# Kernel tuning notes

Measured on AMD Instinct MI355X. Metric: run time of the kernel, lower is better.

Reference implementation:

```python
import jax, jax.numpy as jnp
import numpy as np

HEADS = 8
DIM_HEAD = 32
SCALE = DIM_HEAD ** (-0.5)


def setup_inputs() -> dict:
    key = jax.random.key(0)
    k1, k2, k3, k4 = jax.random.split(key, 4)
    x = jax.random.normal(k1, (16, 256, 64, 64), dtype=jnp.float32)
    # conv 1x1 weights stored as [out_ch, in_ch]
    w_qkv = jax.random.normal(k2, (3 * HEADS * DIM_HEAD, 256), dtype=jnp.float32) * 0.05
    w_out = jax.random.normal(k3, (256, HEADS * DIM_HEAD), dtype=jnp.float32) * 0.05
    b_out = jax.random.normal(k4, (256,), dtype=jnp.float32) * 0.05
    return {"x": x, "w_qkv": w_qkv, "w_out": w_out, "b_out": b_out}


def reference(x, w_qkv, w_out, b_out):
    b, c, h, w = x.shape
    n = h * w
    # 1x1 conv (no bias) == channel matmul
    qkv = jnp.einsum('bchw,oc->bohw', x, w_qkv)            # [b, 3*H*D, h, w]
    qkv = qkv.reshape(b, 3, HEADS, DIM_HEAD, n)            # chunk then 'b (h c) xy'
    q, k, v = qkv[:, 0], qkv[:, 1], qkv[:, 2]              # [b, H, D, n]
    q = jax.nn.softmax(q, axis=-2) * SCALE                 # softmax over channel dim d
    k = jax.nn.softmax(k, axis=-1)                         # softmax over spatial n
    context = jnp.einsum('bhdn,bhen->bhde', k, v)          # [b, H, D, D]
    out = jnp.einsum('bhde,bhdn->bhen', context, q)        # [b, H, D, n]
    out = out.reshape(b, HEADS * DIM_HEAD, h, w)
    # 1x1 conv with bias
    return jnp.einsum('bchw,oc->bohw', out, w_out) + b_out[None, :, None, None]
```

## Files before the change

kernel.cpp:

```cpp
#include <hip/hip_runtime.h>
#include <cstddef>
#include <cstdint>

#define NN 4096
#define CIN 256
#define CQKV 768
#define NBATCH 16
#define QSCALE 0.17677669529663687f

typedef short s16x8 __attribute__((ext_vector_type(8)));
typedef float f32x4 __attribute__((ext_vector_type(4)));

__device__ __forceinline__ float bf2f(unsigned short u) {
    unsigned int x = ((unsigned int)u) << 16;
    return __builtin_bit_cast(float, x);
}
__device__ __forceinline__ unsigned short f2bf(float f) {
    unsigned int u = __builtin_bit_cast(unsigned int, f);
    return (unsigned short)((u + 0x7fffu + ((u >> 16) & 1u)) >> 16);
}
__device__ __forceinline__ void glds16(const void* gsrc, void* lds) {
    __builtin_amdgcn_global_load_lds(
        (const __attribute__((address_space(1))) unsigned int*)gsrc,
        (__attribute__((address_space(3))) unsigned int*)lds,
        16, 0, 0);
}

__global__ __launch_bounds__(256)
void xpose(const float* __restrict__ x, unsigned short* __restrict__ xT)
{
    const int b = blockIdx.z;
    const int n0 = blockIdx.x * 64, c0 = blockIdx.y * 64;
    __shared__ float xs[64][65];
    const int t = threadIdx.x;
    const float* xb = x + (size_t)b * CIN * NN;
#pragma unroll
    for (int p = 0; p < 4; ++p) {
        const int row = p * 16 + (t >> 4);
        const int col = (t & 15) * 4;
        const float4 v = *reinterpret_cast<const float4*>(
            &xb[(size_t)(c0 + row) * NN + n0 + col]);
        xs[col + 0][row] = v.x; xs[col + 1][row] = v.y;
        xs[col + 2][row] = v.z; xs[col + 3][row] = v.w;
    }
    __syncthreads();
    const int n = t >> 2, cch = (t & 3) * 16;
    unsigned short arr[16];
#pragma unroll
    for (int e = 0; e < 16; ++e) arr[e] = f2bf(xs[n][cch + e]);
    unsigned short* dst = xT + ((size_t)b * NN + n0 + n) * 256 + c0 + cch;
    *reinterpret_cast<s16x8*>(&dst[0]) = *reinterpret_cast<s16x8*>(&arr[0]);
    *reinterpret_cast<s16x8*>(&dst[8]) = *reinterpret_cast<s16x8*>(&arr[8]);
}

__global__ __launch_bounds__(256)
void wcvt(const float* __restrict__ w, unsigned short* __restrict__ wb)
{
    const int i = (blockIdx.x * 256 + threadIdx.x) * 4;
    const float4 v = *reinterpret_cast<const float4*>(&w[i]);
    unsigned short a[4] = { f2bf(v.x), f2bf(v.y), f2bf(v.z), f2bf(v.w) };
    *reinterpret_cast<ushort2*>(&wb[i])     = *reinterpret_cast<ushort2*>(&a[0]);
    *reinterpret_cast<ushort2*>(&wb[i + 2]) = *reinterpret_cast<ushort2*>(&a[2]);
}

__device__ __forceinline__ void gemm_core64(const unsigned short* __restrict__ Ab,
                                            const unsigned short* __restrict__ Bb,
                                            int m0, int n0, char* smem,
                                            f32x4 (&acc)[4][4])
{
    const int t = threadIdx.x;
    const int lane = t & 63, w = t >> 6;
    const int lr = lane & 15, lq = lane >> 4;
    const int wr = (w >> 1) * 64, wc = (w & 1) * 64;
    const int srow = t >> 3;
    const int schunk = (t & 7) ^ (srow & 7);
    const int wq = w << 10;
    const int xr = lr & 7;

    char* A0 = smem;          char* B0 = smem + 16384;
    char* A1 = smem + 32768;  char* B1 = smem + 49152;

#define STG(bufA, bufB, k0)                                                     \
    { _Pragma("unroll") for (int i = 0; i < 4; ++i)                             \
        glds16(Ab + (size_t)(m0 + i*32 + srow)*256 + (k0) + schunk*8,           \
               (bufA) + i*4096 + wq);                                           \
      _Pragma("unroll") for (int i = 0; i < 4; ++i)                             \
        glds16(Bb + (size_t)(n0 + i*32 + srow)*256 + (k0) + schunk*8,           \
               (bufB) + i*4096 + wq); }

#define CMP(bufA, bufB)                                                         \
    { s16x8 af[4][2], bfr[4][2];                                                \
      _Pragma("unroll") for (int m = 0; m < 4; ++m) {                           \
        const char* rp = (bufA) + (wr + m*16 + lr)*128;                         \
        af[m][0] = *(const s16x8*)(rp + (((0*4 + lq) ^ xr) << 4));              \
        af[m][1] = *(const s16x8*)(rp + (((1*4 + lq) ^ xr) << 4)); }            \
      _Pragma("unroll") for (int n = 0; n < 4; ++n) {                           \
        const char* rp = (bufB) + (wc + n*16 + lr)*128;                         \
        bfr[n][0] = *(const s16x8*)(rp + (((0*4 + lq) ^ xr) << 4));             \
        bfr[n][1] = *(const s16x8*)(rp + (((1*4 + lq) ^ xr) << 4)); }           \
      _Pragma("unroll") for (int m = 0; m < 4; ++m)                             \
      _Pragma("unroll") for (int n = 0; n < 4; ++n) {                           \
        acc[m][n] = __builtin_amdgcn_mfma_f32_16x16x32_bf16(af[m][0], bfr[n][0], acc[m][n], 0, 0, 0); \
        acc[m][n] = __builtin_amdgcn_mfma_f32_16x16x32_bf16(af[m][1], bfr[n][1], acc[m][n], 0, 0, 0); }}

    STG(A0, B0, 0);
    __syncthreads();
    STG(A1, B1, 64);
    CMP(A0, B0);
    __syncthreads();
    STG(A0, B0, 128);
    CMP(A1, B1);
    __syncthreads();
    STG(A1, B1, 192);
    CMP(A0, B0);
    __syncthreads();
    CMP(A1, B1);
#undef STG
#undef CMP
}

__global__ __launch_bounds__(256, 2)
void qkv_fused(const unsigned short* __restrict__ wb,
               const unsigned short* __restrict__ xT,
               unsigned short* __restrict__ qT,
               float* __restrict__ ctx_part,
               float* __restrict__ z_part)
{
    __shared__ __align__(16) char smem[65536];
    const int nt = blockIdx.x;
    const int ty = blockIdx.y;
    const int b  = blockIdx.z;
    const int t = threadIdx.x;
    const int lane = t & 63, w = t >> 6;
    const int lr = lane & 15, lq = lane >> 4;
    const int wr = (w >> 1) * 64, wc = (w & 1) * 64;
    const int n0 = nt * 128;

    if (ty < 2) {
        const int m0 = ty * 128;
        const unsigned short* Bb = xT + (size_t)b * NN * 256;
        f32x4 acc[4][4] = {};
        gemm_core64(wb, Bb, m0, n0, smem, acc);

        __syncthreads();
        unsigned short (*qs)[136] = (unsigned short (*)[136])smem;
#pragma unroll
        for (int n = 0; n < 4; ++n) {
            const int col = wc + n * 16 + lr;
#pragma unroll
            for (int hp = 0; hp < 2; ++hp) {
                float mx = -1e30f;
#pragma unroll
                for (int u = 0; u < 2; ++u)
#pragma unroll
                    for (int r = 0; r < 4; ++r)
                        mx = fmaxf(mx, acc[hp * 2 + u][n][r]);
                mx = fmaxf(mx, __shfl_xor(mx, 16));
                mx = fmaxf(mx, __shfl_xor(mx, 32));
                float er[2][4];
                float s = 0.f;
#pragma unroll
                for (int u = 0; u < 2; ++u)
#pragma unroll
                    for (int r = 0; r < 4; ++r) {
                        er[u][r] = __expf(acc[hp * 2 + u][n][r] - mx);
                        s += er[u][r];
                    }
                s += __shfl_xor(s, 16);
                s += __shfl_xor(s, 32);
                const float inv = QSCALE / s;
#pragma unroll
                for (int u = 0; u < 2; ++u) {
                    ushort4 pk;
                    pk.x = f2bf(er[u][0] * inv);
                    pk.y = f2bf(er[u][1] * inv);
                    pk.z = f2bf(er[u][2] * inv);
                    pk.w = f2bf(er[u][3] * inv);
                    *(ushort4*)&qs[col][wr + (hp * 2 + u) * 16 + lq * 4] = pk;
                }
            }
        }
        __syncthreads();
        const int nl = t >> 1, half = t & 1;
        const unsigned short* src = &qs[nl][half * 64];
        unsigned short* dst = qT + ((size_t)b * NN + n0 + nl) * 256 + m0 + half * 64;
#pragma unroll
        for (int i = 0; i < 8; ++i)
            *(s16x8*)(dst + i * 8) = *(const s16x8*)(src + i * 8);
    } else {
        const int g = ty - 2;
        const unsigned short* An = xT + ((size_t)b * NN + (size_t)n0) * 256;

        f32x4 acc[4][4] = {};
        gemm_core64(An, wb, 0, 256 + g * 128, smem, acc);

        unsigned int ekpk[4][4][2];
        float zl[4] = {0.f, 0.f, 0.f, 0.f};
#pragma unroll
        for (int m = 0; m < 4; ++m)
#pragma unroll
            for (int nn = 0; nn < 4; ++nn) {
                const unsigned short u0 = f2bf(__expf(acc[m][nn][0]));
                const unsigned short u1 = f2bf(__expf(acc[m][nn][1]));
                const unsigned short u2 = f2bf(__expf(acc[m][nn][2]));
                const unsigned short u3 = f2bf(__expf(acc[m][nn][3]));
                zl[nn] += bf2f(u0) + bf2f(u1) + bf2f(u2) + bf2f(u3);
                ekpk[m][nn][0] = (unsigned int)u0 | ((unsigned int)u1 << 16);
                ekpk[m][nn][1] = (unsigned int)u2 | ((unsigned int)u3 << 16);
            }
#pragma unroll
        for (int nn = 0; nn < 4; ++nn) {
            zl[nn] += __shfl_xor(zl[nn], 16);
            zl[nn] += __shfl_xor(zl[nn], 32);
        }
        const float zv = (lq == 0) ? zl[0] : (lq == 1) ? zl[1] : (lq == 2) ? zl[2] : zl[3];
        z_part[((((size_t)(b * 32 + nt)) * 2 + g) * 2 + (w >> 1)) * 128 + wc + lane] = zv;

#pragma unroll
        for (int m = 0; m < 4; ++m)
#pragma unroll
            for (int nn = 0; nn < 4; ++nn) acc[m][nn] = (f32x4){0.f, 0.f, 0.f, 0.f};
        gemm_core64(An, wb, 0, 512 + g * 128, smem, acc);

        __syncthreads();
#pragma unroll
        for (int m = 0; m < 4; ++m)
#pragma unroll
            for (int nn = 0; nn < 4; ++nn) {
                const int col = wc + nn * 16 + lr;
                const int swz = (col & 7) << 4;
                const int rowb = (wr + m * 16 + lq * 4) * 2;
                *(unsigned int*)(smem + ((col * 256 + rowb) ^ swz))       = ekpk[m][nn][0];
                *(unsigned int*)(smem + ((col * 256 + rowb + 4) ^ swz))   = ekpk[m][nn][1];
                const unsigned int vp0 = (unsigned int)f2bf(acc[m][nn][0])
                                       | ((unsigned int)f2bf(acc[m][nn][1]) << 16);
                const unsigned int vp1 = (unsigned int)f2bf(acc[m][nn][2])
                                       | ((unsigned int)f2bf(acc[m][nn][3]) << 16);
                *(unsigned int*)(smem + 32768 + ((col * 256 + rowb) ^ swz))     = vp0;
                *(unsigned int*)(smem + 32768 + ((col * 256 + rowb + 4) ^ swz)) = vp1;
            }
        __syncthreads();

        f32x4 cacc[2][2] = {};
#pragma unroll
        for (int ks = 0; ks < 4; ++ks) {
            s16x8 af[2], bfv[2];
#pragma unroll
            for (int dt = 0; dt < 2; ++dt) {
                const int drow = w * 32 + dt * 16 + lr;
                af[dt] = *(const s16x8*)(smem +
                    ((drow * 256 + ks * 64 + lq * 16) ^ ((drow & 7) << 4)));
            }
#pragma unroll
            for (int et = 0; et < 2; ++et) {
                const int erow = w * 32 + et * 16 + lr;
                bfv[et] = *(const s16x8*)(smem + 32768 +
                    ((erow * 256 + ks * 64 + lq * 16) ^ ((erow & 7) << 4)));
            }
#pragma unroll
            for (int dt = 0; dt < 2; ++dt)
#pragma unroll
                for (int et = 0; et < 2; ++et)
                    cacc[dt][et] = __builtin_amdgcn_mfma_f32_16x16x32_bf16(
                        af[dt], bfv[et], cacc[dt][et], 0, 0, 0);
        }
        float* cp = ctx_part + ((((size_t)(b * 32 + nt)) * 2 + g) * 4 + w) * 1024;
#pragma unroll
        for (int dt = 0; dt < 2; ++dt)
#pragma unroll
            for (int et = 0; et < 2; ++et)
#pragma unroll
                for (int r = 0; r < 4; ++r)
                    cp[(dt * 16 + lq * 4 + r) * 32 + et * 16 + lr] = cacc[dt][et][r];
    }
}

__global__ __launch_bounds__(256)
void make_m(const float* __restrict__ ctx_part, const float* __restrict__ z_part,
            const float* __restrict__ w_out, unsigned short* __restrict__ Mmat)
{
    const int h = blockIdx.x, b = blockIdx.y;
    const int g = h >> 2, hh = h & 3;
    const int t = threadIdx.x;
    __shared__ float ctx[32][33];
    __shared__ float zinv[32];

    for (int c = t; c < 1024; c += 256) {
        float s = 0.f;
#pragma unroll 8
        for (int nt = 0; nt < 32; ++nt)
            s += ctx_part[((((size_t)(b * 32 + nt)) * 2 + g) * 4 + hh) * 1024 + c];
        ctx[c >> 5][c & 31] = s;
    }
    if (t < 32) {
        float z = 0.f;
#pragma unroll 8
        for (int nt = 0; nt < 32; ++nt) {
            const size_t base = (((size_t)(b * 32 + nt)) * 2 + g) * 2;
            z += z_part[(base + 0) * 128 + hh * 32 + t];
            z += z_part[(base + 1) * 128 + hh * 32 + t];
        }
        zinv[t] = 1.f / z;
    }
    __syncthreads();

    const int o = t;
    float wrow[32];
#pragma unroll
    for (int e = 0; e < 32; ++e)
        wrow[e] = w_out[(size_t)o * 256 + h * 32 + e];
#pragma unroll 4
    for (int d = 0; d < 32; ++d) {
        float s = 0.f;
#pragma unroll
        for (int e = 0; e < 32; ++e)
            s = fmaf(wrow[e], ctx[d][e], s);
        Mmat[((size_t)b * 256 + o) * 256 + h * 32 + d] = f2bf(s * zinv[d]);
    }
}

__global__ __launch_bounds__(256, 2)
void gemm_out(const unsigned short* __restrict__ Mmat,
              const unsigned short* __restrict__ qT,
              float* __restrict__ out, const float* __restrict__ bias)
{
    __shared__ __align__(16) char smem[65536];
    const int bz = blockIdx.z;
    const int m0 = blockIdx.y * 128, n0 = blockIdx.x * 128;
    const unsigned short* Ab = Mmat + (size_t)bz * 256 * 256;
    const unsigned short* Bb = qT + (size_t)bz * NN * 256;

    f32x4 acc[4][4] = {};
    gemm_core64(Ab, Bb, m0, n0, smem, acc);

    const int t = threadIdx.x;
    const int lane = t & 63, w = t >> 6;
    const int lr = lane & 15, lq = lane >> 4;
    const int wr = (w >> 1) * 64, wc = (w & 1) * 64;

    __syncthreads();
#pragma unroll
    for (int m = 0; m < 4; ++m)
#pragma unroll
        for (int r = 0; r < 4; ++r) {
            const int row = wr + m * 16 + lq * 4 + r;
            const float bv = bias[m0 + row];
            const int rb = row * 512;
            const int xs = (row & 7) << 4;
#pragma unroll
            for (int n = 0; n < 4; ++n) {
                const int col = wc + n * 16 + lr;
                *(float*)(smem + rb + ((col * 4) ^ xs)) = acc[m][n][r] + bv;
            }
        }
    __syncthreads();

    float* Yb = out + (size_t)bz * CIN * NN;
#pragma unroll
    for (int p = 0; p < 8; ++p) {
        const int row = p * 16 + (t >> 4);
        const int rb = row * 512;
        const int xs = (row & 7) << 4;
        const int cb = (t & 15) * 32;
        const float4 v0 = *(const float4*)(smem + rb + ((cb + 0) ^ xs));
        const float4 v1 = *(const float4*)(smem + rb + ((cb + 16) ^ xs));
        float* dst = Yb + (size_t)(m0 + row) * NN + n0 + (t & 15) * 8;
        *(float4*)dst = v0;
        *(float4*)(dst + 4) = v1;
    }
}

extern "C" void kernel_launch(void* const* d_in, const int* in_sizes, int n_in,
                              void* d_out, int out_size, void* d_ws, size_t ws_size,
                              hipStream_t stream)
{
    const float* x     = (const float*)d_in[0];
    const float* w_qkv = (const float*)d_in[1];
    const float* w_out = (const float*)d_in[2];
    const float* b_out = (const float*)d_in[3];
    float* out = (float*)d_out;

    char* ws = (char*)d_ws;
    size_t off = 0;
    unsigned short* xT  = (unsigned short*)(ws + off);  off += (size_t)NBATCH * NN * CIN * 2;
    unsigned short* qT  = (unsigned short*)(ws + off);  off += (size_t)NBATCH * NN * CIN * 2;
    float* ctx_part     = (float*)(ws + off);           off += (size_t)NBATCH * 32 * 2 * 4 * 1024 * 4;
    float* z_part       = (float*)(ws + off);           off += (size_t)NBATCH * 32 * 2 * 2 * 128 * 4;
    unsigned short* Mmat= (unsigned short*)(ws + off);  off += (size_t)NBATCH * 256 * 256 * 2;
    unsigned short* wb  = (unsigned short*)(ws + off);  off += (size_t)CQKV * CIN * 2;

    xpose<<<dim3(NN / 64, CIN / 64, NBATCH), 256, 0, stream>>>(x, xT);
    wcvt<<<dim3(CQKV * CIN / 1024), 256, 0, stream>>>(w_qkv, wb);

    qkv_fused<<<dim3(32, 4, NBATCH), 256, 0, stream>>>(wb, xT, qT, ctx_part, z_part);

    make_m<<<dim3(8, NBATCH), 256, 0, stream>>>(ctx_part, z_part, w_out, Mmat);

    gemm_out<<<dim3(32, 2, NBATCH), 256, 0, stream>>>(Mmat, qT, out, b_out);
}
```

Before: 105.0 us.

## Fuse QKV projection into one pass per spatial tile with resident x slab

Replaces the four-way split QKV kernel with a single block per (batch, 128-position tile). That block keeps the whole 128x256 bf16 x slab in LDS and streams six weight tiles through a double buffer, running the Q softmax, K exp/sum and K·V context epilogues in sequence. The aim is to load x once instead of four times and to overlap the weight loads with compute. In exchange it uses 128 KB of dynamic LDS at one block per CU, leaves only 512 blocks in the grid, and rewrites the Q softmax as a row-wise pass over bf16-rounded logits staged in LDS.

```diff
diff --git a/kernel.cpp b/kernel.cpp
--- a/kernel.cpp
+++ b/kernel.cpp
@@ -61,6 +61,243 @@
     unsigned short a[4] = { f2bf(v.x), f2bf(v.y), f2bf(v.z), f2bf(v.w) };
     *reinterpret_cast<ushort2*>(&wb[i])     = *reinterpret_cast<ushort2*>(&a[0]);
     *reinterpret_cast<ushort2*>(&wb[i + 2]) = *reinterpret_cast<ushort2*>(&a[2]);
+}
+
+__global__ __launch_bounds__(256, 1)
+void onepass(const unsigned short* __restrict__ wb,
+             const unsigned short* __restrict__ xT,
+             unsigned short* __restrict__ qT,
+             float* __restrict__ ctx_part,
+             float* __restrict__ z_part)
+{
+    extern __shared__ char smem[];
+    constexpr int BUF0 = 65536, BUF1 = 98304;
+    const int nt = blockIdx.x, b = blockIdx.y;
+    const int n0 = nt * 128;
+    const int t = threadIdx.x;
+    const int lane = t & 63, w = t >> 6;
+    const int lr = lane & 15, lq = lane >> 4;
+    const int wr = (w >> 1) * 64, wc = (w & 1) * 64;
+    const unsigned short* Aslab = xT + ((size_t)b * NN + n0) * 256;
+
+    f32x4 acc[4][4];
+    unsigned int ekpk[4][4][2];
+
+#define ISSUE_A()                                                              \
+  { _Pragma("unroll") for (int i = 0; i < 16; ++i)                             \
+      glds16(Aslab + (size_t)(i * 8 + (t >> 5)) * 256                          \
+                 + ((t & 31) ^ (t >> 5)) * 8,                                  \
+             smem + i * 4096 + (w << 10)); }
+
+#define ISSUE_B(bufoff, trow, kh)                                              \
+  { _Pragma("unroll") for (int i = 0; i < 8; ++i)                              \
+      glds16(wb + (size_t)((trow) + i * 16 + (t >> 4)) * 256 + (kh) * 128      \
+                 + ((t & 15) ^ ((t >> 4) & 7)) * 8,                            \
+             smem + (bufoff) + i * 4096 + (w << 10)); }
+
+#define COMPUTE_HALF(bufbase, gk0)                                             \
+  { _Pragma("unroll") for (int ksl = 0; ksl < 4; ++ksl) {                      \
+      s16x8 af[4], bfr[4];                                                     \
+      _Pragma("unroll") for (int m = 0; m < 4; ++m) {                          \
+          const int row = wr + m * 16 + lr;                                    \
+          af[m] = *(const s16x8*)(smem + row * 512 +                           \
+              (((((gk0) + ksl) * 4 + lq) ^ (row & 7)) << 4)); }                \
+      _Pragma("unroll") for (int nn = 0; nn < 4; ++nn) {                       \
+          const int col = wc + nn * 16 + lr;                                   \
+          bfr[nn] = *(const s16x8*)(smem + (bufbase) + col * 256 +             \
+              (((ksl * 4 + lq) ^ (col & 7)) << 4)); }                          \
+      _Pragma("unroll") for (int m = 0; m < 4; ++m)                            \
+      _Pragma("unroll") for (int nn = 0; nn < 4; ++nn)                         \
+          acc[m][nn] = __builtin_amdgcn_mfma_f32_16x16x32_bf16(                \
+              af[m], bfr[nn], acc[m][nn], 0, 0, 0); } }
+
+#define QEPI(qi)                                                               \
+  { _Pragma("unroll") for (int m = 0; m < 4; ++m)                              \
+    _Pragma("unroll") for (int nn = 0; nn < 4; ++nn)                           \
+    _Pragma("unroll") for (int r = 0; r < 4; ++r) {                            \
+        const int n = wr + m * 16 + lq * 4 + r;                                \
+        const int c = wc + nn * 16 + lr;                                       \
+        *(unsigned short*)(smem + BUF1 +                                       \
+            ((n * 256 + c * 2) ^ ((n & 7) << 4))) = f2bf(acc[m][nn][r]);       \
+    }                                                                          \
+    __syncthreads();                                                           \
+    _Pragma("unroll") for (int rep = 0; rep < 2; ++rep) {                      \
+        const int id = t + rep * 256;                                          \
+        const int nl = id >> 2, hh = id & 3;                                   \
+        const int swz = (nl & 7) << 4;                                         \
+        s16x8 rv[4];                                                           \
+        _Pragma("unroll") for (int i = 0; i < 4; ++i)                          \
+            rv[i] = *(const s16x8*)(smem + BUF1 +                              \
+                ((nl * 256 + hh * 64 + i * 16) ^ swz));                        \
+        float fv[32]; float mx = -1e30f;                                       \
+        _Pragma("unroll") for (int i = 0; i < 4; ++i)                          \
+        _Pragma("unroll") for (int j = 0; j < 8; ++j) {                        \
+            fv[i * 8 + j] = bf2f((unsigned short)rv[i][j]);                    \
+            mx = fmaxf(mx, fv[i * 8 + j]); }                                   \
+        float s = 0.f;                                                         \
+        _Pragma("unroll") for (int k2 = 0; k2 < 32; ++k2) {                    \
+            fv[k2] = __expf(fv[k2] - mx); s += fv[k2]; }                       \
+        const float inv = QSCALE / s;                                          \
+        _Pragma("unroll") for (int i = 0; i < 4; ++i) {                        \
+            s16x8 wv;                                                          \
+            _Pragma("unroll") for (int j = 0; j < 8; ++j)                      \
+                wv[j] = (short)f2bf(fv[i * 8 + j] * inv);                      \
+            *(s16x8*)(smem + BUF1 + ((nl * 256 + hh * 64 + i * 16) ^ swz))     \
+                = wv; }                                                        \
+    }                                                                          \
+    __syncthreads();                                                           \
+    { const int nl = t >> 1, hf = t & 1;                                       \
+      unsigned short* dst = qT + ((size_t)b * NN + n0 + nl) * 256              \
+                            + (qi) * 128 + hf * 64;                            \
+      _Pragma("unroll") for (int i = 0; i < 8; ++i)                            \
+          *(s16x8*)(dst + i * 8) = *(const s16x8*)(smem + BUF1 +               \
+              ((nl * 256 + hf * 128 + i * 16) ^ ((nl & 7) << 4)));             \
+    }                                                                          \
+    __syncthreads(); }
+
+#define KEPI(g)                                                                \
+  { float zl[4] = {0.f, 0.f, 0.f, 0.f};                                        \
+    _Pragma("unroll") for (int m = 0; m < 4; ++m)                              \
+    _Pragma("unroll") for (int nn = 0; nn < 4; ++nn) {                         \
+        const unsigned short u0 = f2bf(__expf(acc[m][nn][0]));                 \
+        const unsigned short u1 = f2bf(__expf(acc[m][nn][1]));                 \
+        const unsigned short u2 = f2bf(__expf(acc[m][nn][2]));                 \
+        const unsigned short u3 = f2bf(__expf(acc[m][nn][3]));                 \
+        zl[nn] += bf2f(u0) + bf2f(u1) + bf2f(u2) + bf2f(u3);                   \
+        ekpk[m][nn][0] = (unsigned int)u0 | ((unsigned int)u1 << 16);          \
+        ekpk[m][nn][1] = (unsigned int)u2 | ((unsigned int)u3 << 16);          \
+    }                                                                          \
+    _Pragma("unroll") for (int nn = 0; nn < 4; ++nn) {                         \
+        zl[nn] += __shfl_xor(zl[nn], 16);                                      \
+        zl[nn] += __shfl_xor(zl[nn], 32); }                                    \
+    const float zv = (lq == 0) ? zl[0] : (lq == 1) ? zl[1]                     \
+                   : (lq == 2) ? zl[2] : zl[3];                                \
+    z_part[((((size_t)(b * 32 + nt)) * 2 + (g)) * 2 + (w >> 1)) * 128          \
+           + wc + lane] = zv; }
+
+#define VEPI(g)                                                                \
+  { f32x4 cacc[2][2] = {};                                                     \
+    _Pragma("unroll") for (int p = 0; p < 2; ++p) {                            \
+        if ((w >> 1) == p) {                                                   \
+            _Pragma("unroll") for (int m = 0; m < 4; ++m)                      \
+            _Pragma("unroll") for (int nn = 0; nn < 4; ++nn) {                 \
+                const int col = wc + nn * 16 + lr;                             \
+                const int swz = (col & 7) << 4;                                \
+                const int rowb = (m * 16 + lq * 4) * 2;                        \
+                *(unsigned int*)(smem + BUF1 + ((col * 128 + rowb) ^ swz))     \
+                    = ekpk[m][nn][0];                                          \
+                *(unsigned int*)(smem + BUF1 + ((col * 128 + rowb + 4) ^ swz)) \
+                    = ekpk[m][nn][1];                                          \
+                const unsigned int vp0 = (unsigned int)f2bf(acc[m][nn][0])     \
+                    | ((unsigned int)f2bf(acc[m][nn][1]) << 16);               \
+                const unsigned int vp1 = (unsigned int)f2bf(acc[m][nn][2])     \
+                    | ((unsigned int)f2bf(acc[m][nn][3]) << 16);               \
+                *(unsigned int*)(smem + BUF1 + 16384 +                         \
+                    ((col * 128 + rowb) ^ swz)) = vp0;                         \
+                *(unsigned int*)(smem + BUF1 + 16384 +                         \
+                    ((col * 128 + rowb + 4) ^ swz)) = vp1;                     \
+            }                                                                  \
+        }                                                                      \
+        __syncthreads();                                                       \
+        _Pragma("unroll") for (int ks2 = 0; ks2 < 2; ++ks2) {                  \
+            s16x8 afk[2], bfv[2];                                              \
+            _Pragma("unroll") for (int dt = 0; dt < 2; ++dt) {                 \
+                const int drow = w * 32 + dt * 16 + lr;                        \
+                afk[dt] = *(const s16x8*)(smem + BUF1 + drow * 128 +           \
+                    ((((ks2 * 4 + lq) ^ (drow & 7))) << 4)); }                 \
+            _Pragma("unroll") for (int et = 0; et < 2; ++et) {                 \
+                const int erow = w * 32 + et * 16 + lr;                        \
+                bfv[et] = *(const s16x8*)(smem + BUF1 + 16384 + erow * 128 +   \
+                    ((((ks2 * 4 + lq) ^ (erow & 7))) << 4)); }                 \
+            _Pragma("unroll") for (int dt = 0; dt < 2; ++dt)                   \
+            _Pragma("unroll") for (int et = 0; et < 2; ++et)                   \
+                cacc[dt][et] = __builtin_amdgcn_mfma_f32_16x16x32_bf16(        \
+                    afk[dt], bfv[et], cacc[dt][et], 0, 0, 0);                  \
+        }                                                                      \
+        __syncthreads();                                                       \
+    }                                                                          \
+    float* cp = ctx_part + ((((size_t)(b * 32 + nt)) * 2 + (g)) * 4 + w) * 1024; \
+    _Pragma("unroll") for (int dt = 0; dt < 2; ++dt)                           \
+    _Pragma("unroll") for (int et = 0; et < 2; ++et)                           \
+    _Pragma("unroll") for (int r = 0; r < 4; ++r)                              \
+        cp[(dt * 16 + lq * 4 + r) * 32 + et * 16 + lr] = cacc[dt][et][r]; }
+
+    const int TROW[6] = {0, 128, 256, 512, 384, 640};
+
+    ISSUE_A();
+    ISSUE_B(BUF0, 0, 0);
+    __syncthreads();
+
+#pragma unroll
+    for (int h = 0; h < 12; ++h) {
+        if ((h & 1) == 0) {
+#pragma unroll
+            for (int m = 0; m < 4; ++m)
+#pragma unroll
+                for (int nn = 0; nn < 4; ++nn)
+                    acc[m][nn] = (f32x4){0.f, 0.f, 0.f, 0.f};
+        }
+        if (h < 11)
+            ISSUE_B((h & 1) ? BUF0 : BUF1, TROW[(h + 1) >> 1], ((h + 1) & 1));
+        COMPUTE_HALF((h & 1) ? BUF1 : BUF0, (h & 1) * 4);
+        __syncthreads();
+        if (h == 1)       { QEPI(0); }
+        else if (h == 3)  { QEPI(1); }
+        else if (h == 5)  { KEPI(0); }
+        else if (h == 7)  { VEPI(0); }
+        else if (h == 9)  { KEPI(1); }
+        else if (h == 11) { VEPI(1); }
+    }
+#undef ISSUE_A
+#undef ISSUE_B
+#undef COMPUTE_HALF
+#undef QEPI
+#undef KEPI
+#undef VEPI
+}
+
+__global__ __launch_bounds__(256)
+void make_m(const float* __restrict__ ctx_part, const float* __restrict__ z_part,
+            const float* __restrict__ w_out, unsigned short* __restrict__ Mmat)
+{
+    const int h = blockIdx.x, b = blockIdx.y;
+    const int g = h >> 2, hh = h & 3;
+    const int t = threadIdx.x;
+    __shared__ float ctx[32][33];
+    __shared__ float zinv[32];
+
+    for (int c = t; c < 1024; c += 256) {
+        float s = 0.f;
+#pragma unroll 8
+        for (int nt = 0; nt < 32; ++nt)
+            s += ctx_part[((((size_t)(b * 32 + nt)) * 2 + g) * 4 + hh) * 1024 + c];
+        ctx[c >> 5][c & 31] = s;
+    }
+    if (t < 32) {
+        float z = 0.f;
+#pragma unroll 8
+        for (int nt = 0; nt < 32; ++nt) {
+            const size_t base = (((size_t)(b * 32 + nt)) * 2 + g) * 2;
+            z += z_part[(base + 0) * 128 + hh * 32 + t];
+            z += z_part[(base + 1) * 128 + hh * 32 + t];
+        }
+        zinv[t] = 1.f / z;
+    }
+    __syncthreads();
+
+    const int o = t;
+    float wrow[32];
+#pragma unroll
+    for (int e = 0; e < 32; ++e)
+        wrow[e] = w_out[(size_t)o * 256 + h * 32 + e];
+#pragma unroll 4
+    for (int d = 0; d < 32; ++d) {
+        float s = 0.f;
+#pragma unroll
+        for (int e = 0; e < 32; ++e)
+            s = fmaf(wrow[e], ctx[d][e], s);
+        Mmat[((size_t)b * 256 + o) * 256 + h * 32 + d] = f2bf(s * zinv[d]);
+    }
 }
 
 __device__ __forceinline__ void gemm_core64(const unsigned short* __restrict__ Ab,
@@ -120,206 +357,6 @@
 }
 
 __global__ __launch_bounds__(256, 2)
-void qkv_fused(const unsigned short* __restrict__ wb,
-               const unsigned short* __restrict__ xT,
-               unsigned short* __restrict__ qT,
-               float* __restrict__ ctx_part,
-               float* __restrict__ z_part)
-{
-    __shared__ __align__(16) char smem[65536];
-    const int nt = blockIdx.x;
-    const int ty = blockIdx.y;
-    const int b  = blockIdx.z;
-    const int t = threadIdx.x;
-    const int lane = t & 63, w = t >> 6;
-    const int lr = lane & 15, lq = lane >> 4;
-    const int wr = (w >> 1) * 64, wc = (w & 1) * 64;
-    const int n0 = nt * 128;
-
-    if (ty < 2) {
-        const int m0 = ty * 128;
-        const unsigned short* Bb = xT + (size_t)b * NN * 256;
-        f32x4 acc[4][4] = {};
-        gemm_core64(wb, Bb, m0, n0, smem, acc);
-
-        __syncthreads();
-        unsigned short (*qs)[136] = (unsigned short (*)[136])smem;
-#pragma unroll
-        for (int n = 0; n < 4; ++n) {
-            const int col = wc + n * 16 + lr;
-#pragma unroll
-            for (int hp = 0; hp < 2; ++hp) {
-                float mx = -1e30f;
-#pragma unroll
-                for (int u = 0; u < 2; ++u)
-#pragma unroll
-                    for (int r = 0; r < 4; ++r)
-                        mx = fmaxf(mx, acc[hp * 2 + u][n][r]);
-                mx = fmaxf(mx, __shfl_xor(mx, 16));
-                mx = fmaxf(mx, __shfl_xor(mx, 32));
-                float er[2][4];
-                float s = 0.f;
-#pragma unroll
-                for (int u = 0; u < 2; ++u)
-#pragma unroll
-                    for (int r = 0; r < 4; ++r) {
-                        er[u][r] = __expf(acc[hp * 2 + u][n][r] - mx);
-                        s += er[u][r];
-                    }
-                s += __shfl_xor(s, 16);
-                s += __shfl_xor(s, 32);
-                const float inv = QSCALE / s;
-#pragma unroll
-                for (int u = 0; u < 2; ++u) {
-                    ushort4 pk;
-                    pk.x = f2bf(er[u][0] * inv);
-                    pk.y = f2bf(er[u][1] * inv);
-                    pk.z = f2bf(er[u][2] * inv);
-                    pk.w = f2bf(er[u][3] * inv);
-                    *(ushort4*)&qs[col][wr + (hp * 2 + u) * 16 + lq * 4] = pk;
-                }
-            }
-        }
-        __syncthreads();
-        const int nl = t >> 1, half = t & 1;
-        const unsigned short* src = &qs[nl][half * 64];
-        unsigned short* dst = qT + ((size_t)b * NN + n0 + nl) * 256 + m0 + half * 64;
-#pragma unroll
-        for (int i = 0; i < 8; ++i)
-            *(s16x8*)(dst + i * 8) = *(const s16x8*)(src + i * 8);
-    } else {
-        const int g = ty - 2;
-        const unsigned short* An = xT + ((size_t)b * NN + (size_t)n0) * 256;
-
-        f32x4 acc[4][4] = {};
-        gemm_core64(An, wb, 0, 256 + g * 128, smem, acc);
-
-        unsigned int ekpk[4][4][2];
-        float zl[4] = {0.f, 0.f, 0.f, 0.f};
-#pragma unroll
-        for (int m = 0; m < 4; ++m)
-#pragma unroll
-            for (int nn = 0; nn < 4; ++nn) {
-                const unsigned short u0 = f2bf(__expf(acc[m][nn][0]));
-                const unsigned short u1 = f2bf(__expf(acc[m][nn][1]));
-                const unsigned short u2 = f2bf(__expf(acc[m][nn][2]));
-                const unsigned short u3 = f2bf(__expf(acc[m][nn][3]));
-                zl[nn] += bf2f(u0) + bf2f(u1) + bf2f(u2) + bf2f(u3);
-                ekpk[m][nn][0] = (unsigned int)u0 | ((unsigned int)u1 << 16);
-                ekpk[m][nn][1] = (unsigned int)u2 | ((unsigned int)u3 << 16);
-            }
-#pragma unroll
-        for (int nn = 0; nn < 4; ++nn) {
-            zl[nn] += __shfl_xor(zl[nn], 16);
-            zl[nn] += __shfl_xor(zl[nn], 32);
-        }
-        const float zv = (lq == 0) ? zl[0] : (lq == 1) ? zl[1] : (lq == 2) ? zl[2] : zl[3];
-        z_part[((((size_t)(b * 32 + nt)) * 2 + g) * 2 + (w >> 1)) * 128 + wc + lane] = zv;
-
-#pragma unroll
-        for (int m = 0; m < 4; ++m)
-#pragma unroll
-            for (int nn = 0; nn < 4; ++nn) acc[m][nn] = (f32x4){0.f, 0.f, 0.f, 0.f};
-        gemm_core64(An, wb, 0, 512 + g * 128, smem, acc);
-
-        __syncthreads();
-#pragma unroll
-        for (int m = 0; m < 4; ++m)
-#pragma unroll
-            for (int nn = 0; nn < 4; ++nn) {
-                const int col = wc + nn * 16 + lr;
-                const int swz = (col & 7) << 4;
-                const int rowb = (wr + m * 16 + lq * 4) * 2;
-                *(unsigned int*)(smem + ((col * 256 + rowb) ^ swz))       = ekpk[m][nn][0];
-                *(unsigned int*)(smem + ((col * 256 + rowb + 4) ^ swz))   = ekpk[m][nn][1];
-                const unsigned int vp0 = (unsigned int)f2bf(acc[m][nn][0])
-                                       | ((unsigned int)f2bf(acc[m][nn][1]) << 16);
-                const unsigned int vp1 = (unsigned int)f2bf(acc[m][nn][2])
-                                       | ((unsigned int)f2bf(acc[m][nn][3]) << 16);
-                *(unsigned int*)(smem + 32768 + ((col * 256 + rowb) ^ swz))     = vp0;
-                *(unsigned int*)(smem + 32768 + ((col * 256 + rowb + 4) ^ swz)) = vp1;
-            }
-        __syncthreads();
-
-        f32x4 cacc[2][2] = {};
-#pragma unroll
-        for (int ks = 0; ks < 4; ++ks) {
-            s16x8 af[2], bfv[2];
-#pragma unroll
-            for (int dt = 0; dt < 2; ++dt) {
-                const int drow = w * 32 + dt * 16 + lr;
-                af[dt] = *(const s16x8*)(smem +
-                    ((drow * 256 + ks * 64 + lq * 16) ^ ((drow & 7) << 4)));
-            }
-#pragma unroll
-            for (int et = 0; et < 2; ++et) {
-                const int erow = w * 32 + et * 16 + lr;
-                bfv[et] = *(const s16x8*)(smem + 32768 +
-                    ((erow * 256 + ks * 64 + lq * 16) ^ ((erow & 7) << 4)));
-            }
-#pragma unroll
-            for (int dt = 0; dt < 2; ++dt)
-#pragma unroll
-                for (int et = 0; et < 2; ++et)
-                    cacc[dt][et] = __builtin_amdgcn_mfma_f32_16x16x32_bf16(
-                        af[dt], bfv[et], cacc[dt][et], 0, 0, 0);
-        }
-        float* cp = ctx_part + ((((size_t)(b * 32 + nt)) * 2 + g) * 4 + w) * 1024;
-#pragma unroll
-        for (int dt = 0; dt < 2; ++dt)
-#pragma unroll
-            for (int et = 0; et < 2; ++et)
-#pragma unroll
-                for (int r = 0; r < 4; ++r)
-                    cp[(dt * 16 + lq * 4 + r) * 32 + et * 16 + lr] = cacc[dt][et][r];
-    }
-}
-
-__global__ __launch_bounds__(256)
-void make_m(const float* __restrict__ ctx_part, const float* __restrict__ z_part,
-            const float* __restrict__ w_out, unsigned short* __restrict__ Mmat)
-{
-    const int h = blockIdx.x, b = blockIdx.y;
-    const int g = h >> 2, hh = h & 3;
-    const int t = threadIdx.x;
-    __shared__ float ctx[32][33];
-    __shared__ float zinv[32];
-
-    for (int c = t; c < 1024; c += 256) {
-        float s = 0.f;
-#pragma unroll 8
-        for (int nt = 0; nt < 32; ++nt)
-            s += ctx_part[((((size_t)(b * 32 + nt)) * 2 + g) * 4 + hh) * 1024 + c];
-        ctx[c >> 5][c & 31] = s;
-    }
-    if (t < 32) {
-        float z = 0.f;
-#pragma unroll 8
-        for (int nt = 0; nt < 32; ++nt) {
-            const size_t base = (((size_t)(b * 32 + nt)) * 2 + g) * 2;
-            z += z_part[(base + 0) * 128 + hh * 32 + t];
-            z += z_part[(base + 1) * 128 + hh * 32 + t];
-        }
-        zinv[t] = 1.f / z;
-    }
-    __syncthreads();
-
-    const int o = t;
-    float wrow[32];
-#pragma unroll
-    for (int e = 0; e < 32; ++e)
-        wrow[e] = w_out[(size_t)o * 256 + h * 32 + e];
-#pragma unroll 4
-    for (int d = 0; d < 32; ++d) {
-        float s = 0.f;
-#pragma unroll
-        for (int e = 0; e < 32; ++e)
-            s = fmaf(wrow[e], ctx[d][e], s);
-        Mmat[((size_t)b * 256 + o) * 256 + h * 32 + d] = f2bf(s * zinv[d]);
-    }
-}
-
-__global__ __launch_bounds__(256, 2)
 void gemm_out(const unsigned short* __restrict__ Mmat,
               const unsigned short* __restrict__ qT,
               float* __restrict__ out, const float* __restrict__ bias)
@@ -392,7 +429,7 @@
     xpose<<<dim3(NN / 64, CIN / 64, NBATCH), 256, 0, stream>>>(x, xT);
     wcvt<<<dim3(CQKV * CIN / 1024), 256, 0, stream>>>(w_qkv, wb);
 
-    qkv_fused<<<dim3(32, 4, NBATCH), 256, 0, stream>>>(wb, xT, qT, ctx_part, z_part);
+    onepass<<<dim3(32, NBATCH), 256, 131072, stream>>>(wb, xT, qT, ctx_part, z_part);
 
     make_m<<<dim3(8, NBATCH), 256, 0, stream>>>(ctx_part, z_part, w_out, Mmat);
 
```

After: 126.5 us. +20.5%, slower.

## Replace double-buffered GEMM core with four-stage K=32 pipeline using vmcnt waits

Applied to the files above, without the earlier changes.

Rewrites the shared GEMM mainloop from a two-buffer K=64 schedule with full __syncthreads to a four-slot ring of K=32 stages, issuing three stages ahead. It waits on explicit vmcnt counts plus raw s_barrier so global-to-LDS loads stay in flight across compute steps. It also raises wave priority around the MFMA bursts and uses a new XOR swizzle for 64-byte rows. The aim is to hide load latency better, at the cost of more barriers and a correctness dependence on the hand-tuned waitcnt counts.

```diff
diff --git a/kernel.cpp b/kernel.cpp
--- a/kernel.cpp
+++ b/kernel.cpp
@@ -63,60 +63,60 @@
     *reinterpret_cast<ushort2*>(&wb[i + 2]) = *reinterpret_cast<ushort2*>(&a[2]);
 }
 
-__device__ __forceinline__ void gemm_core64(const unsigned short* __restrict__ Ab,
-                                            const unsigned short* __restrict__ Bb,
-                                            int m0, int n0, char* smem,
-                                            f32x4 (&acc)[4][4])
+__device__ __forceinline__ void gemm_pipe(const unsigned short* __restrict__ Ab,
+                                          const unsigned short* __restrict__ Bb,
+                                          int m0, int n0, char* smem,
+                                          f32x4 (&acc)[4][4])
 {
     const int t = threadIdx.x;
     const int lane = t & 63, w = t >> 6;
     const int lr = lane & 15, lq = lane >> 4;
     const int wr = (w >> 1) * 64, wc = (w & 1) * 64;
-    const int srow = t >> 3;
-    const int schunk = (t & 7) ^ (srow & 7);
-    const int wq = w << 10;
-    const int xr = lr & 7;
-
-    char* A0 = smem;          char* B0 = smem + 16384;
-    char* A1 = smem + 32768;  char* B1 = smem + 49152;
-
-#define STG(bufA, bufB, k0)                                                     \
-    { _Pragma("unroll") for (int i = 0; i < 4; ++i)                             \
-        glds16(Ab + (size_t)(m0 + i*32 + srow)*256 + (k0) + schunk*8,           \
-               (bufA) + i*4096 + wq);                                           \
-      _Pragma("unroll") for (int i = 0; i < 4; ++i)                             \
-        glds16(Bb + (size_t)(n0 + i*32 + srow)*256 + (k0) + schunk*8,           \
-               (bufB) + i*4096 + wq); }
-
-#define CMP(bufA, bufB)                                                         \
-    { s16x8 af[4][2], bfr[4][2];                                                \
-      _Pragma("unroll") for (int m = 0; m < 4; ++m) {                           \
-        const char* rp = (bufA) + (wr + m*16 + lr)*128;                         \
-        af[m][0] = *(const s16x8*)(rp + (((0*4 + lq) ^ xr) << 4));              \
-        af[m][1] = *(const s16x8*)(rp + (((1*4 + lq) ^ xr) << 4)); }            \
-      _Pragma("unroll") for (int n = 0; n < 4; ++n) {                           \
-        const char* rp = (bufB) + (wc + n*16 + lr)*128;                         \
-        bfr[n][0] = *(const s16x8*)(rp + (((0*4 + lq) ^ xr) << 4));             \
-        bfr[n][1] = *(const s16x8*)(rp + (((1*4 + lq) ^ xr) << 4)); }           \
-      _Pragma("unroll") for (int m = 0; m < 4; ++m)                             \
-      _Pragma("unroll") for (int n = 0; n < 4; ++n) {                           \
-        acc[m][n] = __builtin_amdgcn_mfma_f32_16x16x32_bf16(af[m][0], bfr[n][0], acc[m][n], 0, 0, 0); \
-        acc[m][n] = __builtin_amdgcn_mfma_f32_16x16x32_bf16(af[m][1], bfr[n][1], acc[m][n], 0, 0, 0); }}
-
-    STG(A0, B0, 0);
-    __syncthreads();
-    STG(A1, B1, 64);
-    CMP(A0, B0);
-    __syncthreads();
-    STG(A0, B0, 128);
-    CMP(A1, B1);
-    __syncthreads();
-    STG(A1, B1, 192);
-    CMP(A0, B0);
-    __syncthreads();
-    CMP(A1, B1);
-#undef STG
-#undef CMP
+    const int ch0 = (w * 2 + 0) * 64 + lane;
+    const int ch1 = (w * 2 + 1) * 64 + lane;
+    const int r0 = ch0 >> 2, c0s = (ch0 & 3) ^ ((r0 >> 1) & 3);
+    const int r1 = ch1 >> 2, c1s = (ch1 & 3) ^ ((r1 >> 1) & 3);
+    char* Abuf = smem;
+    char* Bbuf = smem + 32768;
+
+#define STG_H(h)                                                               \
+  { char* ab = Abuf + ((h) & 3) * 8192;                                        \
+    char* bb = Bbuf + ((h) & 3) * 8192;                                        \
+    glds16(Ab + (size_t)(m0 + r0) * 256 + (h) * 32 + c0s * 8, ab + (w*2+0)*1024); \
+    glds16(Ab + (size_t)(m0 + r1) * 256 + (h) * 32 + c1s * 8, ab + (w*2+1)*1024); \
+    glds16(Bb + (size_t)(n0 + r0) * 256 + (h) * 32 + c0s * 8, bb + (w*2+0)*1024); \
+    glds16(Bb + (size_t)(n0 + r1) * 256 + (h) * 32 + c1s * 8, bb + (w*2+1)*1024); }
+
+#define CMP_H(h)                                                               \
+  { char* ab = Abuf + ((h) & 3) * 8192;                                        \
+    char* bb = Bbuf + ((h) & 3) * 8192;                                        \
+    s16x8 af[4], bfr[4];                                                       \
+    _Pragma("unroll") for (int m = 0; m < 4; ++m) {                            \
+        const int row = wr + m * 16 + lr;                                      \
+        af[m] = *(const s16x8*)(ab + row * 64 + ((lq ^ ((row >> 1) & 3)) << 4)); } \
+    _Pragma("unroll") for (int n = 0; n < 4; ++n) {                            \
+        const int col = wc + n * 16 + lr;                                      \
+        bfr[n] = *(const s16x8*)(bb + col * 64 + ((lq ^ ((col >> 1) & 3)) << 4)); } \
+    __builtin_amdgcn_s_setprio(1);                                             \
+    _Pragma("unroll") for (int m = 0; m < 4; ++m)                              \
+    _Pragma("unroll") for (int n = 0; n < 4; ++n)                              \
+        acc[m][n] = __builtin_amdgcn_mfma_f32_16x16x32_bf16(af[m], bfr[n],     \
+                                                            acc[m][n], 0, 0, 0); \
+    __builtin_amdgcn_s_setprio(0); }
+
+    STG_H(0); STG_H(1); STG_H(2);
+#pragma unroll
+    for (int i = 0; i < 8; ++i) {
+        if (i < 6)       asm volatile("s_waitcnt vmcnt(8)" ::: "memory");
+        else if (i == 6) asm volatile("s_waitcnt vmcnt(4)" ::: "memory");
+        else             asm volatile("s_waitcnt vmcnt(0)" ::: "memory");
+        __builtin_amdgcn_s_barrier();
+        __builtin_amdgcn_sched_barrier(0);
+        if (i < 5) STG_H(i + 3);
+        CMP_H(i);
+    }
+#undef STG_H
+#undef CMP_H
 }
 
 __global__ __launch_bounds__(256, 2)
@@ -140,7 +140,7 @@
         const int m0 = ty * 128;
         const unsigned short* Bb = xT + (size_t)b * NN * 256;
         f32x4 acc[4][4] = {};
-        gemm_core64(wb, Bb, m0, n0, smem, acc);
+        gemm_pipe(wb, Bb, m0, n0, smem, acc);
 
         __syncthreads();
         unsigned short (*qs)[136] = (unsigned short (*)[136])smem;
@@ -192,7 +192,7 @@
         const unsigned short* An = xT + ((size_t)b * NN + (size_t)n0) * 256;
 
         f32x4 acc[4][4] = {};
-        gemm_core64(An, wb, 0, 256 + g * 128, smem, acc);
+        gemm_pipe(An, wb, 0, 256 + g * 128, smem, acc);
 
         unsigned int ekpk[4][4][2];
         float zl[4] = {0.f, 0.f, 0.f, 0.f};
@@ -220,7 +220,7 @@
         for (int m = 0; m < 4; ++m)
 #pragma unroll
             for (int nn = 0; nn < 4; ++nn) acc[m][nn] = (f32x4){0.f, 0.f, 0.f, 0.f};
-        gemm_core64(An, wb, 0, 512 + g * 128, smem, acc);
+        gemm_pipe(An, wb, 0, 512 + g * 128, smem, acc);
 
         __syncthreads();
 #pragma unroll
@@ -331,7 +331,7 @@
     const unsigned short* Bb = qT + (size_t)bz * NN * 256;
 
     f32x4 acc[4][4] = {};
-    gemm_core64(Ab, Bb, m0, n0, smem, acc);
+    gemm_pipe(Ab, Bb, m0, n0, smem, acc);
 
     const int t = threadIdx.x;
     const int lane = t & 63, w = t >> 6;
```

New measurement: 107.3 us. 2.2% more time.
